# Optimization experiments

Hardware: AMD Instinct MI355X
Metric: run time of the kernel (lower is better)

## Reference

```python
import jax, jax.numpy as jnp
import numpy as np

DIM = 768
HEADS = 12
DIM_HEAD = 64
ROPE_BASE = 8192.0
LN_EPS = 1e-5


def setup_inputs() -> dict:
    key = jax.random.key(0)
    k1, k2, k3, k4 = jax.random.split(key, 4)
    B, N = 4, 2048
    x = jax.random.normal(k1, (B, N, DIM), dtype=jnp.float32)
    # 2D (time, pitch) coordinates in [0, 64)
    coords = jax.random.uniform(k2, (B, N, 2), dtype=jnp.float32) * 64.0
    ln_gamma = jnp.ones((DIM,), dtype=jnp.float32)
    ln_beta = jnp.zeros((DIM,), dtype=jnp.float32)
    w_qkv = jax.random.normal(k3, (3 * HEADS * DIM_HEAD, DIM), dtype=jnp.float32) * (DIM ** -0.5)
    w_out = jax.random.normal(k4, (DIM, HEADS * DIM_HEAD), dtype=jnp.float32) * ((HEADS * DIM_HEAD) ** -0.5)
    return {"x": x, "coords": coords, "ln_gamma": ln_gamma, "ln_beta": ln_beta,
            "w_qkv": w_qkv, "w_out": w_out}


def _rotate(t, cos, sin):
    # t: [B,H,N,ad]; cos/sin: [B,1,N,ad//2]
    t1 = t[..., 0::2]
    t2 = t[..., 1::2]
    return jnp.concatenate([t1 * cos - t2 * sin, t1 * sin + t2 * cos], axis=-1)


def _axis_cos_sin(coord, axis_dim):
    # coord: [B,N] -> cos/sin: [B,1,N,axis_dim//2]
    half = axis_dim // 2
    exp = jnp.arange(half, dtype=jnp.float32) / half
    inv_freq = jnp.exp(-exp * jnp.log(jnp.float32(ROPE_BASE)))  # [half]
    freqs = coord[:, :, None] * inv_freq[None, None, :]  # [B,N,half]
    return jnp.cos(freqs)[:, None], jnp.sin(freqs)[:, None]


def reference(x, coords, ln_gamma, ln_beta, w_qkv, w_out):
    B, N, D = x.shape
    scale = DIM_HEAD ** -0.5

    # LayerNorm
    mu = jnp.mean(x, axis=-1, keepdims=True)
    var = jnp.mean((x - mu) ** 2, axis=-1, keepdims=True)
    xn = (x - mu) * jax.lax.rsqrt(var + LN_EPS) * ln_gamma + ln_beta

    # QKV projection: [B,N,3*H*dh]
    qkv = jnp.einsum('bnd,ed->bne', xn, w_qkv)
    q, k, v = jnp.split(qkv, 3, axis=-1)

    def to_heads(t):
        return t.reshape(B, N, HEADS, DIM_HEAD).transpose(0, 2, 1, 3)  # b h n d
    q, k, v = to_heads(q), to_heads(k), to_heads(v)

    # 2D axial RoPE: x-axis on dims [0:dh//2), y-axis on dims [dh//2:dh)
    half = DIM_HEAD // 2
    slices = [(0, (0, half)), (1, (half, DIM_HEAD))]
    for axis_idx, (lo, hi) in slices:
        cos, sin = _axis_cos_sin(coords[..., axis_idx], hi - lo)
        q = jnp.concatenate([q[..., :lo], _rotate(q[..., lo:hi], cos, sin), q[..., hi:]], axis=-1)
        k = jnp.concatenate([k[..., :lo], _rotate(k[..., lo:hi], cos, sin), k[..., hi:]], axis=-1)

    # Attention
    dots = jnp.einsum('bhnd,bhmd->bhnm', q, k) * scale
    attn = jax.nn.softmax(dots, axis=-1)
    out = jnp.einsum('bhnm,bhmd->bhnd', attn, v)
    out = out.transpose(0, 2, 1, 3).reshape(B, N, HEADS * DIM_HEAD)
    return jnp.einsum('bne,de->bnd', out, w_out)
```

## Files before the change

### kernel.cpp

```cpp
#include <hip/hip_runtime.h>

#define B_ 4
#define N_ 2048
#define D_ 768
#define H_ 12
#define DH_ 64
#define ROWS_ (B_*N_)
#define E3_ (3*D_)

typedef _Float16 f16;
typedef __attribute__((ext_vector_type(8))) _Float16 half8;
typedef __attribute__((ext_vector_type(4))) _Float16 half4;
typedef __attribute__((ext_vector_type(4))) float floatx4;

__device__ __forceinline__ void gload_lds16(const void* g, void* lds){
  __builtin_amdgcn_global_load_lds(
      (const __attribute__((address_space(1))) unsigned int*)g,
      (__attribute__((address_space(3))) unsigned int*)lds, 16, 0, 0);
}

__global__ __launch_bounds__(256) void cvt_kernel(const float* __restrict__ srcA,
    f16* __restrict__ dstA, int n8a, const float* __restrict__ srcB,
    f16* __restrict__ dstB, int n8b){
  int i = blockIdx.x*256 + threadIdx.x;
  const float* src; f16* dst; int j;
  if (i < n8a){ src = srcA; dst = dstA; j = i; }
  else { j = i - n8a; if (j >= n8b) return; src = srcB; dst = dstB; }
  float4 a = ((const float4*)src)[2*j];
  float4 b = ((const float4*)src)[2*j+1];
  half8 h;
  h[0]=(f16)a.x; h[1]=(f16)a.y; h[2]=(f16)a.z; h[3]=(f16)a.w;
  h[4]=(f16)b.x; h[5]=(f16)b.y; h[6]=(f16)b.z; h[7]=(f16)b.w;
  *(half8*)(dst + (size_t)j*8) = h;
}

__global__ __launch_bounds__(256) void ln_kernel(const float* __restrict__ x,
    const float* __restrict__ g, const float* __restrict__ be, f16* __restrict__ xn){
  int w = threadIdx.x >> 6, lane = threadIdx.x & 63;
  int row = blockIdx.x*4 + w;
  const float* xr = x + (size_t)row * D_;
  int c = lane*4;
  float4 f0 = *(const float4*)(xr + c);
  float4 f1 = *(const float4*)(xr + c + 256);
  float4 f2 = *(const float4*)(xr + c + 512);
  float s  = (f0.x+f0.y+f0.z+f0.w) + (f1.x+f1.y+f1.z+f1.w) + (f2.x+f2.y+f2.z+f2.w);
  float ss = (f0.x*f0.x+f0.y*f0.y+f0.z*f0.z+f0.w*f0.w)
           + (f1.x*f1.x+f1.y*f1.y+f1.z*f1.z+f1.w*f1.w)
           + (f2.x*f2.x+f2.y*f2.y+f2.z*f2.z+f2.w*f2.w);
  #pragma unroll
  for(int off=1; off<64; off<<=1){
    s  += __shfl_xor(s,  off, 64);
    ss += __shfl_xor(ss, off, 64);
  }
  float mean = s * (1.0f/D_);
  float var  = ss * (1.0f/D_) - mean*mean;
  float rstd = rsqrtf(var + 1e-5f);
  f16* xo = xn + (size_t)row * D_;
  #pragma unroll
  for(int part=0; part<3; ++part){
    float4 v = part==0 ? f0 : (part==1 ? f1 : f2);
    float4 gg = *(const float4*)(g  + c + part*256);
    float4 bb = *(const float4*)(be + c + part*256);
    half4 o;
    o[0] = (f16)((v.x-mean)*rstd*gg.x + bb.x);
    o[1] = (f16)((v.y-mean)*rstd*gg.y + bb.y);
    o[2] = (f16)((v.z-mean)*rstd*gg.z + bb.z);
    o[3] = (f16)((v.w-mean)*rstd*gg.w + bb.w);
    *(half4*)(xo + c + part*256) = o;
  }
}

__global__ __launch_bounds__(256) void rope_tab_kernel(const float* __restrict__ coords,
    float* __restrict__ T){
  int i = blockIdx.x*256 + threadIdx.x;
  int token = i >> 5, ax = (i >> 4) & 1, m = i & 15;
  float coord = coords[(size_t)token*2 + ax];
  float fr = exp2f((float)m * (-13.0f/16.0f));
  float sn, cs;
  sincosf(coord * fr, &sn, &cs);
  T[(size_t)token*64 + ax*32 + m]      = cs;
  T[(size_t)token*64 + ax*32 + 16 + m] = sn;
}

__global__ __launch_bounds__(256) void qkv_gemm(const f16* __restrict__ A,
    const f16* __restrict__ W, const float* __restrict__ T,
    f16* __restrict__ Q, f16* __restrict__ Kt, f16* __restrict__ VT){
  __shared__ __align__(16) char smem[128*136*2];
  f16* sA = (f16*)smem;
  f16* sB = (f16*)(smem + 8192);
  f16* sT = (f16*)smem;
  int tid = threadIdx.x;
  int w = tid >> 6, lane = tid & 63, quad = lane >> 4, l15 = lane & 15;
  int row0 = blockIdx.y * 128;
  int e0   = blockIdx.x * 128;
  int wr = (w >> 1) * 64, wc = (w & 1) * 64;
  int r0c = tid >> 2,        ci0 = (tid & 3) * 8;
  int r1c = (256+tid) >> 2,  ci1 = (tid & 3) * 8;
  floatx4 acc[4][4];
  #pragma unroll
  for(int i=0;i<4;++i)
    #pragma unroll
    for(int j=0;j<4;++j) acc[i][j] = (floatx4){0.f,0.f,0.f,0.f};

  for(int k0=0; k0<D_; k0+=32){
    __syncthreads();
    gload_lds16(A + (size_t)(row0+r0c)*D_ + k0 + ci0, sA + (size_t)(w*64)*8);
    gload_lds16(A + (size_t)(row0+r1c)*D_ + k0 + ci1, sA + (size_t)(256 + w*64)*8);
    gload_lds16(W + (size_t)(e0 +r0c)*D_ + k0 + ci0, sB + (size_t)(w*64)*8);
    gload_lds16(W + (size_t)(e0 +r1c)*D_ + k0 + ci1, sB + (size_t)(256 + w*64)*8);
    __syncthreads();
    half8 af[4], bf[4];
    #pragma unroll
    for(int mi=0;mi<4;++mi) af[mi] = *(const half8*)&sA[(wr + mi*16 + l15)*32 + quad*8];
    #pragma unroll
    for(int ni=0;ni<4;++ni) bf[ni] = *(const half8*)&sB[(wc + ni*16 + l15)*32 + quad*8];
    #pragma unroll
    for(int mi=0;mi<4;++mi)
      #pragma unroll
      for(int ni=0;ni<4;++ni)
        acc[mi][ni] = __builtin_amdgcn_mfma_f32_16x16x32_f16(af[mi], bf[ni], acc[mi][ni], 0, 0, 0);
  }
  int part = e0 / D_;
  int erel = e0 % D_;
  if (part == 2){
    #pragma unroll
    for(int ni=0;ni<4;++ni){
      int col = erel + wc + ni*16 + l15;
      int h = col >> 6, d = col & 63;
      #pragma unroll
      for(int mi=0;mi<4;++mi){
        int rbase = row0 + wr + mi*16 + quad*4;
        int b = rbase >> 11, n = rbase & 2047;
        half4 h4;
        #pragma unroll
        for(int reg=0;reg<4;++reg) h4[reg] = (f16)acc[mi][ni][reg];
        *(half4*)&VT[(((size_t)b*H_ + h)*DH_ + d)*N_ + n] = h4;
      }
    }
    return;
  }
  __syncthreads();
  #pragma unroll
  for(int mi=0;mi<4;++mi){
    int r = wr + mi*16 + quad*4;
    #pragma unroll
    for(int ni=0;ni<4;++ni){
      int c = wc + ni*16 + l15;
      #pragma unroll
      for(int reg=0;reg<4;++reg)
        sT[(size_t)(r+reg)*136 + c] = (f16)acc[mi][ni][reg];
    }
  }
  __syncthreads();
  int r  = tid >> 1;
  int hh = tid & 1;
  int n_global = row0 + r;
  const float* tt = T + (size_t)n_global*64;
  float tv[64];
  #pragma unroll
  for(int j=0;j<16;++j) *(float4*)&tv[j*4] = *(const float4*)(tt + j*4);
  f16 v[64];
  #pragma unroll
  for(int j=0;j<8;++j) *(half8*)&v[j*8] = *(const half8*)&sT[(size_t)r*136 + hh*64 + j*8];
  f16 o[64];
  #pragma unroll
  for(int ax=0; ax<2; ++ax){
    #pragma unroll
    for(int m=0;m<16;++m){
      float cs = tv[ax*32 + m];
      float sn = tv[ax*32 + 16 + m];
      float t1 = (float)v[ax*32 + 2*m];
      float t2 = (float)v[ax*32 + 2*m + 1];
      o[ax*32 + m]      = (f16)(t1*cs - t2*sn);
      o[ax*32 + 16 + m] = (f16)(t1*sn + t2*cs);
    }
  }
  int h = erel/64 + hh;
  int b = n_global >> 11, n = n_global & 2047;
  f16* dst = (part==0) ? Q : Kt;
  f16* op = dst + (((size_t)b*H_ + h)*N_ + n)*DH_;
  #pragma unroll
  for(int j=0;j<8;++j) *(half8*)(op + j*8) = *(half8*)&o[j*8];
}

__global__ __launch_bounds__(256) void attn_kernel(const f16* __restrict__ Q,
    const f16* __restrict__ K, const f16* __restrict__ VT, f16* __restrict__ AO){
  __shared__ f16 sV[2][64*64];
  __shared__ f16 sP[4][2][16*64];
  int bh = blockIdx.y;
  int q0 = blockIdx.x * 128;
  int tid = threadIdx.x;
  int w = tid >> 6, lane = tid & 63, quad = lane >> 4, l15 = lane & 15;
  const f16* Qb = Q  + (size_t)bh*N_*DH_;
  const f16* Ks = K  + (size_t)bh*N_*DH_;
  const f16* Vb = VT + (size_t)bh*DH_*N_;

  int sd = tid >> 2, sc = tid & 3;
  const f16* vsrc = Vb + (size_t)sd*N_ + sc*16;
  int sw0 = sd*64 + (((2*sc    ) ^ (sd & 7)) << 3);
  int sw1 = sd*64 + (((2*sc + 1) ^ (sd & 7)) << 3);

  half8 qf0[2], qf1[2];
  #pragma unroll
  for(int s2=0;s2<2;++s2){
    const f16* qrow = Qb + (size_t)(q0 + 32*w + 16*s2 + l15)*DH_ + quad*8;
    qf0[s2] = *(const half8*)(qrow);
    qf1[s2] = *(const half8*)(qrow + 32);
    half8 cs8;
    #pragma unroll
    for(int j=0;j<8;++j) cs8[j] = (f16)0.18033688f;
    qf0[s2] = qf0[s2] * cs8;
    qf1[s2] = qf1[s2] * cs8;
  }

  half8 kf0[4], kf1[4];
  #pragma unroll
  for(int nt=0;nt<4;++nt){
    const f16* krow = Ks + (size_t)(16*nt + l15)*DH_ + quad*8;
    kf0[nt] = *(const half8*)(krow);
    kf1[nt] = *(const half8*)(krow + 32);
  }

  {
    half8 g0 = *(const half8*)(vsrc);
    half8 g1 = *(const half8*)(vsrc + 8);
    *(half8*)&sV[0][sw0] = g0;
    *(half8*)&sV[0][sw1] = g1;
  }

  float l_run[2] = {0.0f, 0.0f};
  floatx4 acc[2][4];
  #pragma unroll
  for(int s2=0;s2<2;++s2)
    #pragma unroll
    for(int dt=0;dt<4;++dt) acc[s2][dt] = (floatx4){0.f,0.f,0.f,0.f};
  __syncthreads();

  f16* Prow[2] = { &sP[w][0][l15*64], &sP[w][1][l15*64] };
  int vsw = (l15 & 7);

  const floatx4 SINIT = (floatx4){-8.f,-8.f,-8.f,-8.f};
  int ph = 0;
  for(int kv0=0; kv0<N_; kv0+=64, ph^=1){
    int kvn = kv0 + 64; if (kvn >= N_) kvn = 0;
    half8 g0 = *(const half8*)(vsrc + kvn);
    half8 g1 = *(const half8*)(vsrc + kvn + 8);
    floatx4 s[2][4];
    #pragma unroll
    for(int s2=0;s2<2;++s2)
      #pragma unroll
      for(int nt=0; nt<4; ++nt){
        floatx4 z = SINIT;
        z = __builtin_amdgcn_mfma_f32_16x16x32_f16(kf0[nt], qf0[s2], z, 0, 0, 0);
        z = __builtin_amdgcn_mfma_f32_16x16x32_f16(kf1[nt], qf1[s2], z, 0, 0, 0);
        s[s2][nt] = z;
      }
    #pragma unroll
    for(int nt=0;nt<4;++nt){
      const f16* krow = Ks + (size_t)(kvn + 16*nt + l15)*DH_ + quad*8;
      kf0[nt] = *(const half8*)(krow);
      kf1[nt] = *(const half8*)(krow + 32);
    }
    #pragma unroll
    for(int s2=0;s2<2;++s2){
      f16* Pb = Prow[s2];
      float r4[4];
      #pragma unroll
      for(int nt=0;nt<4;++nt){
        float p0 = exp2f(s[s2][nt][0]);
        float p1 = exp2f(s[s2][nt][1]);
        float p2 = exp2f(s[s2][nt][2]);
        float p3 = exp2f(s[s2][nt][3]);
        half4 h;
        h[0]=(f16)p0; h[1]=(f16)p1; h[2]=(f16)p2; h[3]=(f16)p3;
        *(half4*)&Pb[((4*nt + quad) ^ l15) << 2] = h;
        r4[nt] = (p0+p1)+(p2+p3);
      }
      l_run[s2] += (r4[0]+r4[1])+(r4[2]+r4[3]);
    }
    {
      const f16* sv = &sV[ph][0];
      half4 a0a = *(const half4*)&Prow[0][((2*quad    ) ^ l15) << 2];
      half4 a1a = *(const half4*)&Prow[0][((2*quad + 1) ^ l15) << 2];
      half4 b0a = *(const half4*)&Prow[0][((8 + 2*quad    ) ^ l15) << 2];
      half4 b1a = *(const half4*)&Prow[0][((8 + 2*quad + 1) ^ l15) << 2];
      half4 a0b = *(const half4*)&Prow[1][((2*quad    ) ^ l15) << 2];
      half4 a1b = *(const half4*)&Prow[1][((2*quad + 1) ^ l15) << 2];
      half4 b0b = *(const half4*)&Prow[1][((8 + 2*quad    ) ^ l15) << 2];
      half4 b1b = *(const half4*)&Prow[1][((8 + 2*quad + 1) ^ l15) << 2];
      half8 pf0a = __builtin_shufflevector(a0a, a1a, 0,1,2,3,4,5,6,7);
      half8 pf1a = __builtin_shufflevector(b0a, b1a, 0,1,2,3,4,5,6,7);
      half8 pf0b = __builtin_shufflevector(a0b, a1b, 0,1,2,3,4,5,6,7);
      half8 pf1b = __builtin_shufflevector(b0b, b1b, 0,1,2,3,4,5,6,7);
      #pragma unroll
      for(int dt=0;dt<4;++dt){
        int rr = 16*dt + l15;
        half8 v0 = *(const half8*)&sv[rr*64 + (((quad    ) ^ vsw) << 3)];
        half8 v1 = *(const half8*)&sv[rr*64 + (((quad + 4) ^ vsw) << 3)];
        acc[0][dt] = __builtin_amdgcn_mfma_f32_16x16x32_f16(v0, pf0a, acc[0][dt], 0, 0, 0);
        acc[0][dt] = __builtin_amdgcn_mfma_f32_16x16x32_f16(v1, pf1a, acc[0][dt], 0, 0, 0);
        acc[1][dt] = __builtin_amdgcn_mfma_f32_16x16x32_f16(v0, pf0b, acc[1][dt], 0, 0, 0);
        acc[1][dt] = __builtin_amdgcn_mfma_f32_16x16x32_f16(v1, pf1b, acc[1][dt], 0, 0, 0);
      }
    }
    {
      f16* dstv = &sV[ph^1][0];
      *(half8*)&dstv[sw0] = g0;
      *(half8*)&dstv[sw1] = g1;
    }
    __syncthreads();
  }
  int b = bh / H_, h = bh % H_;
  #pragma unroll
  for(int s2=0;s2<2;++s2){
    float l = l_run[s2];
    l += __shfl_xor(l, 16, 64);
    l += __shfl_xor(l, 32, 64);
    float inv = 1.0f / l;
    f16* Pb = Prow[s2];
    #pragma unroll
    for(int dt=0;dt<4;++dt){
      half4 h4;
      h4[0]=(f16)(acc[s2][dt][0]*inv); h4[1]=(f16)(acc[s2][dt][1]*inv);
      h4[2]=(f16)(acc[s2][dt][2]*inv); h4[3]=(f16)(acc[s2][dt][3]*inv);
      *(half4*)&Pb[((4*dt + quad) ^ l15) << 2] = h4;
    }
    half4 c0 = *(const half4*)&Pb[((4*quad    ) ^ l15) << 2];
    half4 c1 = *(const half4*)&Pb[((4*quad + 1) ^ l15) << 2];
    half4 c2 = *(const half4*)&Pb[((4*quad + 2) ^ l15) << 2];
    half4 c3 = *(const half4*)&Pb[((4*quad + 3) ^ l15) << 2];
    half8 o0 = __builtin_shufflevector(c0, c1, 0,1,2,3,4,5,6,7);
    half8 o1 = __builtin_shufflevector(c2, c3, 0,1,2,3,4,5,6,7);
    f16* op = AO + ((size_t)(b*N_ + q0 + 32*w + 16*s2 + l15))*D_ + h*DH_ + quad*16;
    *(half8*)(op)     = o0;
    *(half8*)(op + 8) = o1;
  }
}

__global__ __launch_bounds__(256) void out_gemm(const f16* __restrict__ A,
    const f16* __restrict__ W, float* __restrict__ C){
  __shared__ f16 sA[128*32];
  __shared__ f16 sB[128*32];
  int tid = threadIdx.x;
  int w = tid >> 6, lane = tid & 63, quad = lane >> 4, l15 = lane & 15;
  int row0 = blockIdx.y * 128;
  int e0   = blockIdx.x * 128;
  int wr = (w >> 1) * 64, wc = (w & 1) * 64;
  int r0c = tid >> 2,        ci0 = (tid & 3) * 8;
  int r1c = (256+tid) >> 2,  ci1 = (tid & 3) * 8;
  floatx4 acc[4][4];
  #pragma unroll
  for(int i=0;i<4;++i)
    #pragma unroll
    for(int j=0;j<4;++j) acc[i][j] = (floatx4){0.f,0.f,0.f,0.f};

  for(int k0=0; k0<D_; k0+=32){
    __syncthreads();
    gload_lds16(A + (size_t)(row0+r0c)*D_ + k0 + ci0, sA + (size_t)(w*64)*8);
    gload_lds16(A + (size_t)(row0+r1c)*D_ + k0 + ci1, sA + (size_t)(256 + w*64)*8);
    gload_lds16(W + (size_t)(e0 +r0c)*D_ + k0 + ci0, sB + (size_t)(w*64)*8);
    gload_lds16(W + (size_t)(e0 +r1c)*D_ + k0 + ci1, sB + (size_t)(256 + w*64)*8);
    __syncthreads();
    half8 af[4], bf[4];
    #pragma unroll
    for(int mi=0;mi<4;++mi) af[mi] = *(const half8*)&sA[(wr + mi*16 + l15)*32 + quad*8];
    #pragma unroll
    for(int ni=0;ni<4;++ni) bf[ni] = *(const half8*)&sB[(wc + ni*16 + l15)*32 + quad*8];
    #pragma unroll
    for(int mi=0;mi<4;++mi)
      #pragma unroll
      for(int ni=0;ni<4;++ni)
        acc[mi][ni] = __builtin_amdgcn_mfma_f32_16x16x32_f16(af[mi], bf[ni], acc[mi][ni], 0, 0, 0);
  }
  #pragma unroll
  for(int ni=0;ni<4;++ni){
    int col = e0 + wc + ni*16 + l15;
    #pragma unroll
    for(int mi=0;mi<4;++mi){
      int rbase = row0 + wr + mi*16 + quad*4;
      #pragma unroll
      for(int reg=0;reg<4;++reg)
        C[(size_t)(rbase+reg)*D_ + col] = acc[mi][ni][reg];
    }
  }
}

extern "C" void kernel_launch(void* const* d_in, const int* in_sizes, int n_in,
                              void* d_out, int out_size, void* d_ws, size_t ws_size,
                              hipStream_t stream) {
  (void)in_sizes; (void)n_in; (void)out_size; (void)ws_size;
  const float* x      = (const float*)d_in[0];
  const float* coords = (const float*)d_in[1];
  const float* g      = (const float*)d_in[2];
  const float* be     = (const float*)d_in[3];
  const float* wqkv   = (const float*)d_in[4];
  const float* wout   = (const float*)d_in[5];
  float* out = (float*)d_out;
  char* ws = (char*)d_ws;
  const size_t SEG = (size_t)ROWS_ * D_ * 2;
  f16* xn  = (f16*)(ws + 0*SEG);
  f16* Q   = (f16*)(ws + 1*SEG);
  f16* K   = (f16*)(ws + 2*SEG);
  f16* VT  = (f16*)(ws + 3*SEG);
  f16* AO  = (f16*)(ws + 4*SEG);
  f16* W16 = (f16*)(ws + 5*SEG);
  f16* Wo16= (f16*)(ws + 5*SEG + (size_t)E3_*D_*2);
  float* T = (float*)AO;

  const int n8a = E3_*D_/8, n8b = D_*D_/8;
  cvt_kernel <<<(n8a+n8b+255)/256, 256, 0, stream>>>(wqkv, W16, n8a, wout, Wo16, n8b);
  ln_kernel  <<<ROWS_/4, 256, 0, stream>>>(x, g, be, xn);
  rope_tab_kernel<<<(B_*N_*32)/256, 256, 0, stream>>>(coords, T);
  qkv_gemm   <<<dim3(E3_/128, ROWS_/128), 256, 0, stream>>>(xn, W16, T, Q, K, VT);
  attn_kernel<<<dim3(N_/128, B_*H_), 256, 0, stream>>>(Q, K, VT, AO);
  out_gemm   <<<dim3(D_/128, ROWS_/128), 256, 0, stream>>>(AO, Wo16, out);
}
```

Measured before the change: 283.7 us.

## Stage K tiles through double-buffered shared memory in attention kernel

Each wave previously loaded its own K fragments directly from global memory, so the four waves in a block fetched the same 64x64 K tile redundantly. Now the block cooperatively loads each K tile once into a swizzled, double-buffered LDS buffer alongside V and reads the fragments from LDS. The launch bounds also request 3 blocks per CU. This adds 16KB of LDS per block and extra LDS reads per iteration, and the occupancy hint may force register spilling.

```diff
diff --git a/kernel.cpp b/kernel.cpp
--- a/kernel.cpp
+++ b/kernel.cpp
@@ -183,8 +183,9 @@
   for(int j=0;j<8;++j) *(half8*)(op + j*8) = *(half8*)&o[j*8];
 }
 
-__global__ __launch_bounds__(256) void attn_kernel(const f16* __restrict__ Q,
+__global__ __launch_bounds__(256, 3) void attn_kernel(const f16* __restrict__ Q,
     const f16* __restrict__ K, const f16* __restrict__ VT, f16* __restrict__ AO){
+  __shared__ f16 sK[2][64*64];
   __shared__ f16 sV[2][64*64];
   __shared__ f16 sP[4][2][16*64];
   int bh = blockIdx.y;
@@ -197,6 +198,7 @@
 
   int sd = tid >> 2, sc = tid & 3;
   const f16* vsrc = Vb + (size_t)sd*N_ + sc*16;
+  const f16* ksrc = Ks + (size_t)sd*DH_ + sc*16;
   int sw0 = sd*64 + (((2*sc    ) ^ (sd & 7)) << 3);
   int sw1 = sd*64 + (((2*sc + 1) ^ (sd & 7)) << 3);
 
@@ -213,19 +215,13 @@
     qf1[s2] = qf1[s2] * cs8;
   }
 
-  half8 kf0[4], kf1[4];
-  #pragma unroll
-  for(int nt=0;nt<4;++nt){
-    const f16* krow = Ks + (size_t)(16*nt + l15)*DH_ + quad*8;
-    kf0[nt] = *(const half8*)(krow);
-    kf1[nt] = *(const half8*)(krow + 32);
-  }
-
   {
+    half8 k0 = *(const half8*)(ksrc);
+    half8 k1 = *(const half8*)(ksrc + 8);
     half8 g0 = *(const half8*)(vsrc);
     half8 g1 = *(const half8*)(vsrc + 8);
-    *(half8*)&sV[0][sw0] = g0;
-    *(half8*)&sV[0][sw1] = g1;
+    *(half8*)&sK[0][sw0] = k0;  *(half8*)&sK[0][sw1] = k1;
+    *(half8*)&sV[0][sw0] = g0;  *(half8*)&sV[0][sw1] = g1;
   }
 
   float l_run[2] = {0.0f, 0.0f};
@@ -243,8 +239,18 @@
   int ph = 0;
   for(int kv0=0; kv0<N_; kv0+=64, ph^=1){
     int kvn = kv0 + 64; if (kvn >= N_) kvn = 0;
-    half8 g0 = *(const half8*)(vsrc + kvn);
-    half8 g1 = *(const half8*)(vsrc + kvn + 8);
+    half8 nk0 = *(const half8*)(ksrc + (size_t)kvn*DH_);
+    half8 nk1 = *(const half8*)(ksrc + (size_t)kvn*DH_ + 8);
+    half8 ng0 = *(const half8*)(vsrc + kvn);
+    half8 ng1 = *(const half8*)(vsrc + kvn + 8);
+    const f16* sk = &sK[ph][0];
+    half8 kf0[4], kf1[4];
+    #pragma unroll
+    for(int nt=0;nt<4;++nt){
+      int rr = 16*nt + l15;
+      kf0[nt] = *(const half8*)&sk[rr*64 + (((quad    ) ^ vsw) << 3)];
+      kf1[nt] = *(const half8*)&sk[rr*64 + (((quad + 4) ^ vsw) << 3)];
+    }
     floatx4 s[2][4];
     #pragma unroll
     for(int s2=0;s2<2;++s2)
@@ -255,12 +261,6 @@
         z = __builtin_amdgcn_mfma_f32_16x16x32_f16(kf1[nt], qf1[s2], z, 0, 0, 0);
         s[s2][nt] = z;
       }
-    #pragma unroll
-    for(int nt=0;nt<4;++nt){
-      const f16* krow = Ks + (size_t)(kvn + 16*nt + l15)*DH_ + quad*8;
-      kf0[nt] = *(const half8*)(krow);
-      kf1[nt] = *(const half8*)(krow + 32);
-    }
     #pragma unroll
     for(int s2=0;s2<2;++s2){
       f16* Pb = Prow[s2];
@@ -304,9 +304,10 @@
       }
     }
     {
-      f16* dstv = &sV[ph^1][0];
-      *(half8*)&dstv[sw0] = g0;
-      *(half8*)&dstv[sw1] = g1;
+      f16* dk = &sK[ph^1][0];
+      f16* dv = &sV[ph^1][0];
+      *(half8*)&dk[sw0] = nk0;  *(half8*)&dk[sw1] = nk1;
+      *(half8*)&dv[sw0] = ng0;  *(half8*)&dv[sw1] = ng1;
     }
     __syncthreads();
   }
```

Result: faster. 258.3 us (-9.0%).
